# Kernel tuning notes

Hardware: AMD Instinct MI355X
Metric: run time of the kernel (lower is better)

## Reference

```python
import jax, jax.numpy as jnp
import numpy as np

KS = 7
DIM = 1024
HEADS = 16
B = 2048

def _rpb_index(ks):
    # Replicates the torch buffer: relative_position_index, shape [ks*ks, ks*ks]
    ch = np.arange(ks)
    coords = np.stack(np.meshgrid(ch, ch, indexing='ij')).reshape(2, -1)  # [2, N]
    rel = coords[:, :, None] - coords[:, None, :]                          # [2, N, N]
    rel = rel.transpose(1, 2, 0).copy()                                    # [N, N, 2]
    rel[:, :, 0] += ks - 1
    rel[:, :, 1] += ks - 1
    rel[:, :, 0] *= 2 * ks - 1
    idx = np.flipud(np.fliplr(rel.sum(-1)))
    return jnp.asarray(idx.copy())

def setup_inputs() -> dict:
    key = jax.random.key(0)
    ks = jax.random.split(key, 4)
    x = jax.random.normal(ks[0], (B, KS, KS, DIM), dtype=jnp.float32)
    qkv_w = jax.random.normal(ks[1], (3 * DIM, DIM), dtype=jnp.float32) * (DIM ** -0.5)
    qkv_b = jnp.zeros((3 * DIM,), dtype=jnp.float32)
    rpb = jax.random.normal(ks[2], (HEADS, 2 * KS - 1, 2 * KS - 1), dtype=jnp.float32) * 0.02
    proj_w = jax.random.normal(ks[3], (DIM, DIM), dtype=jnp.float32) * (DIM ** -0.5)
    proj_b = jnp.zeros((DIM,), dtype=jnp.float32)
    return {"x": x, "qkv_w": qkv_w, "qkv_b": qkv_b, "rpb": rpb, "proj_w": proj_w, "proj_b": proj_b}

def reference(x, qkv_w, qkv_b, rpb, proj_w, proj_b):
    Bn, H, W, C = x.shape
    ksz = H
    N = H * W
    heads = rpb.shape[0]
    hd = C // heads
    scale = hd ** -0.5
    idx = _rpb_index(ksz)  # [N, N] int

    qkv = x.reshape(Bn, N, C) @ qkv_w.T + qkv_b              # [B, N, 3C]
    qkv = qkv.reshape(Bn, N, 3, heads, hd).transpose(2, 0, 3, 1, 4)  # [3, B, h, N, hd]
    q, k, v = qkv[0] * scale, qkv[1], qkv[2]

    attn = jnp.einsum('bhnd,bhmd->bhnm', q, k)               # [B, h, N, N]
    # gather relative-position bias: rpb[h, 2k-1, 2k-1] -> flat [(2k-1)^2, h] -> [N, N, h]
    bias = rpb.transpose(1, 2, 0).reshape(-1, heads)[idx.reshape(-1)]
    bias = bias.reshape(N, N, heads).transpose(2, 0, 1)      # [h, N, N]
    attn = jax.nn.softmax(attn + bias[None], axis=-1)

    out = jnp.einsum('bhnm,bhmd->bhnd', attn, v)             # [B, h, N, hd]
    out = out.transpose(0, 2, 1, 3).reshape(Bn, H, W, C)
    return out @ proj_w.T + proj_b
```

## Files before the change

kernel.cpp:

```cpp
#include <hip/hip_runtime.h>


typedef _Float16 f16;
typedef _Float16 f16x8 __attribute__((ext_vector_type(8)));
typedef _Float16 f16x4 __attribute__((ext_vector_type(4)));
typedef float f32x4 __attribute__((ext_vector_type(4)));

#define G1P(p) ((const __attribute__((address_space(1))) unsigned int*)(p))
#define L3P(p) ((__attribute__((address_space(3))) unsigned int*)(p))

__global__ void cvt_kernel(const float* __restrict__ in, f16* __restrict__ out, int n4) {
  int i = blockIdx.x * blockDim.x + threadIdx.x;
  int stride = gridDim.x * blockDim.x;
  const float4* in4 = (const float4*)in;
  f16x4* out4 = (f16x4*)out;
  for (; i < n4; i += stride) {
    float4 v = in4[i];
    f16x4 o = { (f16)v.x, (f16)v.y, (f16)v.z, (f16)v.w };
    out4[i] = o;
  }
}

__global__ void bias_kernel(const float* __restrict__ rpb, f16* __restrict__ bias_t) {
  int h = blockIdx.x;
  for (int e = threadIdx.x; e < 4096; e += blockDim.x) {
    int m = e >> 6, n = e & 63;
    float v = -60000.f;
    if (n < 49 && m < 49) {
      int in_ = n / 7, jn = n % 7, im = m / 7, jm = m % 7;
      v = rpb[h * 169 + (im - in_ + 6) * 13 + (jm - jn + 6)] * 1.44269504f;
    }
    bias_t[h * 4096 + e] = (f16)v;
  }
}

#define VM4 asm volatile("s_waitcnt vmcnt(4)" ::: "memory")
#define VM0 asm volatile("s_waitcnt vmcnt(0)" ::: "memory")
#define NOVM ((void)0)
#define NOSTG ((void)0)

#define STAGE(GB, ROW0, COL0, LDSOFF)                                              \
  {                                                                                \
    const f16* s0_ = (GB) + (size_t)((ROW0) + wid * 32 + srow) * K + ((COL0) + sce); \
    __builtin_amdgcn_global_load_lds(G1P(s0_), L3P(lds + (LDSOFF) + wid * 2048), 16, 0, 0); \
    const f16* s1_ = s0_ + (size_t)16 * K;                                         \
    __builtin_amdgcn_global_load_lds(G1P(s1_), L3P(lds + (LDSOFF) + wid * 2048 + 1024), 16, 0, 0); \
  }

#define MFMA4(AREG, ROW)                                                           \
  acc[ROW][0] = __builtin_amdgcn_mfma_f32_16x16x32_f16(AREG, b0, acc[ROW][0], 0, 0, 0); \
  acc[ROW][1] = __builtin_amdgcn_mfma_f32_16x16x32_f16(AREG, b1, acc[ROW][1], 0, 0, 0); \
  acc[ROW][2] = __builtin_amdgcn_mfma_f32_16x16x32_f16(AREG, b2, acc[ROW][2], 0, 0, 0); \
  acc[ROW][3] = __builtin_amdgcn_mfma_f32_16x16x32_f16(AREG, b3, acc[ROW][3], 0, 0, 0);

#define PHASE(ABASE, BBASE, MH, STG, VMW)                                          \
  {                                                                                \
    f16x8 a0 = *(const f16x8*)((ABASE) + (wm * 128 + (MH) * 64 +  0 + l15) * 64 + swz); \
    f16x8 a1 = *(const f16x8*)((ABASE) + (wm * 128 + (MH) * 64 + 16 + l15) * 64 + swz); \
    f16x8 a2 = *(const f16x8*)((ABASE) + (wm * 128 + (MH) * 64 + 32 + l15) * 64 + swz); \
    f16x8 a3 = *(const f16x8*)((ABASE) + (wm * 128 + (MH) * 64 + 48 + l15) * 64 + swz); \
    if ((MH) == 0) {                                                               \
      b0 = *(const f16x8*)((BBASE) + (wn * 64 +  0 + l15) * 64 + swz);             \
      b1 = *(const f16x8*)((BBASE) + (wn * 64 + 16 + l15) * 64 + swz);             \
      b2 = *(const f16x8*)((BBASE) + (wn * 64 + 32 + l15) * 64 + swz);             \
      b3 = *(const f16x8*)((BBASE) + (wn * 64 + 48 + l15) * 64 + swz);             \
    }                                                                              \
    STG;                                                                           \
    __builtin_amdgcn_s_barrier();                                                  \
    asm volatile("s_waitcnt lgkmcnt(0)" ::: "memory");                             \
    __builtin_amdgcn_sched_barrier(0);                                             \
    __builtin_amdgcn_s_setprio(1);                                                 \
    MFMA4(a0, (MH) * 4 + 0) MFMA4(a1, (MH) * 4 + 1)                                \
    MFMA4(a2, (MH) * 4 + 2) MFMA4(a3, (MH) * 4 + 3)                                \
    __builtin_amdgcn_s_setprio(0);                                                 \
    VMW;                                                                           \
    __builtin_amdgcn_s_barrier();                                                  \
  }

template <typename OutT, bool HB>
__global__ __launch_bounds__(512, 2)
void gemm256(const f16* __restrict__ A, const f16* __restrict__ B,
             const float* __restrict__ bias, OutT* __restrict__ C,
             int N, int K, int ntiles_n) {
  __shared__ char lds[131072];
  const int tid = threadIdx.x;
  const int wid = tid >> 6, ln = tid & 63;
  const int l15 = ln & 15, lhi = ln >> 4;
  const int wm = wid >> 2, wn = wid & 3;
  const int srow = ln >> 2;
  const int sce = (((ln & 3) ^ ((ln >> 3) & 3)) << 3);
  const int swz = ((lhi ^ ((l15 >> 1) & 3)) << 4);

  const int nblk = gridDim.x;
  const int wg = (blockIdx.x & 7) * (nblk >> 3) + (blockIdx.x >> 3);
  const int bn = wg % ntiles_n, bm = wg / ntiles_n;
  const int m0 = bm * 256, n0 = bn * 256;

  f32x4 acc[8][4];
#pragma unroll
  for (int i = 0; i < 8; ++i)
#pragma unroll
    for (int j = 0; j < 4; ++j) acc[i][j] = (f32x4){0.f, 0.f, 0.f, 0.f};
  f16x8 b0, b1, b2, b3;

  STAGE(A, m0, 0, 0);
  STAGE(B, n0, 0, 32768);
  STAGE(A, m0, 32, 16384);
  STAGE(B, n0, 32, 49152);
  STAGE(A, m0, 64, 65536);
  STAGE(B, n0, 64, 98304);
  VM4;
  __builtin_amdgcn_s_barrier();

  for (int i = 0; i < 7; ++i) {
    const int cT1k1 = (2 * i + 1) * 64 + 32;
    const int cT2k0 = (2 * i + 2) * 64;
    const int cT2k1 = cT2k0 + 32;
    const int cT3k0 = (2 * i + 3) * 64;
    PHASE(lds + 0,      lds + 32768,  0, STAGE(A, m0, cT1k1, 81920),  NOVM);
    PHASE(lds + 0,      lds + 32768,  1, STAGE(B, n0, cT1k1, 114688), NOVM);
    PHASE(lds + 16384,  lds + 49152,  0, STAGE(A, m0, cT2k0, 0),      NOVM);
    PHASE(lds + 16384,  lds + 49152,  1, STAGE(B, n0, cT2k0, 32768),  VM4);
    PHASE(lds + 65536,  lds + 98304,  0, STAGE(A, m0, cT2k1, 16384),  NOVM);
    PHASE(lds + 65536,  lds + 98304,  1, STAGE(B, n0, cT2k1, 49152),  NOVM);
    PHASE(lds + 81920,  lds + 114688, 0, STAGE(A, m0, cT3k0, 65536),  NOVM);
    PHASE(lds + 81920,  lds + 114688, 1, STAGE(B, n0, cT3k0, 98304),  VM4);
  }
  PHASE(lds + 0,      lds + 32768,  0, STAGE(A, m0, 15 * 64 + 32, 81920),  NOVM);
  PHASE(lds + 0,      lds + 32768,  1, STAGE(B, n0, 15 * 64 + 32, 114688), NOVM);
  PHASE(lds + 16384,  lds + 49152,  0, NOSTG, NOVM);
  PHASE(lds + 16384,  lds + 49152,  1, NOSTG, VM0);
  PHASE(lds + 65536,  lds + 98304,  0, NOSTG, NOVM);
  PHASE(lds + 65536,  lds + 98304,  1, NOSTG, NOVM);
  PHASE(lds + 81920,  lds + 114688, 0, NOSTG, NOVM);
  PHASE(lds + 81920,  lds + 114688, 1, NOSTG, NOVM);

  float bv[4];
#pragma unroll
  for (int j = 0; j < 4; ++j) bv[j] = bias[n0 + wn * 64 + j * 16 + l15];
#pragma unroll
  for (int ii = 0; ii < 8; ++ii)
#pragma unroll
    for (int r = 0; r < 4; ++r) {
      int gr = m0 + wm * 128 + ii * 16 + lhi * 4 + r;
      if (HB) {
        int bw = gr / 49, n = gr - bw * 49;
#pragma unroll
        for (int j = 0; j < 4; ++j) {
          int gc = n0 + wn * 64 + j * 16 + l15;
          int which = gc >> 10, rem = gc & 1023;
          int h = rem >> 6, d = rem & 63;
          size_t addr = (((size_t)bw * 16 + h) * 3 + which) * 3136 + n * 64 + d;
          C[addr] = (OutT)(acc[ii][j][r] + bv[j]);
        }
      } else {
#pragma unroll
        for (int j = 0; j < 4; ++j) {
          int gc = n0 + wn * 64 + j * 16 + l15;
          C[(size_t)gr * N + gc] = (OutT)(acc[ii][j][r] + bv[j]);
        }
      }
    }
}

__global__ __launch_bounds__(64)
void attn_kernel(const f16* __restrict__ qkv,
                 const f16* __restrict__ bias_t,
                 f16* __restrict__ out) {
  __shared__ char lds[16384];
  const int bh = blockIdx.x;
  const int b = bh >> 4, h = bh & 15;
  const int ln = threadIdx.x;
  const int l15 = ln & 15, lhi = ln >> 4;
  const size_t base = (size_t)b * 49;
  const size_t qb = (size_t)bh * 3 * 3136;
  const size_t kb = qb + 3136;
  const size_t vb = qb + 6272;

  {
    int rA = ln >> 3, lc = ln & 7;
#pragma unroll
    for (int c = 0; c < 8; ++c) {
      int r = c * 8 + rA;
      int rc = r > 48 ? 48 : r;
      int ce = (lc ^ (r & 7)) << 3;
      const f16* g = qkv + kb + rc * 64 + ce;
      __builtin_amdgcn_global_load_lds(G1P(g), L3P(lds + c * 1024), 16, 0, 0);
    }
  }

  int rv = ln > 48 ? 48 : ln;
  const f16* vp = qkv + vb + rv * 64;
  f16x8 vr[8];
#pragma unroll
  for (int j = 0; j < 8; ++j) vr[j] = *(const f16x8*)(vp + j * 8);

  f16x8 qf[4][2];
#pragma unroll
  for (int t = 0; t < 4; ++t) {
    int rq = t * 16 + l15;
    if (rq > 48) rq = 48;
    const f16* qp = qkv + qb + rq * 64 + lhi * 8;
    qf[t][0] = *(const f16x8*)(qp);
    qf[t][1] = *(const f16x8*)(qp + 32);
  }

  const f16* bb = bias_t + h * 4096;
  f16x4 bq[4][4];
#pragma unroll
  for (int i = 0; i < 4; ++i)
#pragma unroll
    for (int j = 0; j < 4; ++j)
      bq[i][j] = *(const f16x4*)(bb + (j * 16 + l15) * 64 + i * 16 + lhi * 4);

#pragma unroll
  for (int d = 0; d < 64; ++d)
    *(f16*)(lds + 8192 + d * 128 + ((ln * 2) ^ ((d & 7) << 4))) = vr[d >> 3][d & 7];

  asm volatile("s_waitcnt vmcnt(0)" ::: "memory");
  __builtin_amdgcn_sched_barrier(0);

  f32x4 acc[4][4];
#pragma unroll
  for (int i = 0; i < 4; ++i)
#pragma unroll
    for (int j = 0; j < 4; ++j) acc[i][j] = (f32x4){0.f, 0.f, 0.f, 0.f};
#pragma unroll
  for (int kk = 0; kk < 2; ++kk) {
    f16x8 bf[4];
#pragma unroll
    for (int t = 0; t < 4; ++t) {
      int mr = t * 16 + l15;
      int pb = (kk * 64 + lhi * 16) ^ ((mr & 7) << 4);
      bf[t] = *(const f16x8*)(lds + mr * 128 + pb);
    }
    __builtin_amdgcn_s_setprio(1);
#pragma unroll
    for (int i = 0; i < 4; ++i)
#pragma unroll
      for (int j = 0; j < 4; ++j)
        acc[i][j] = __builtin_amdgcn_mfma_f32_16x16x32_f16(qf[i][kk], bf[j], acc[i][j], 0, 0, 0);
    __builtin_amdgcn_s_setprio(0);
  }

  const float SC = 0.125f * 1.44269504f;
#pragma unroll
  for (int i = 0; i < 4; ++i) {
#pragma unroll
    for (int r = 0; r < 4; ++r) {
      int n = i * 16 + lhi * 4 + r;
      float lv[4];
#pragma unroll
      for (int j = 0; j < 4; ++j)
        lv[j] = acc[i][j][r] * SC + (float)bq[i][j][r];
      float Mx = fmaxf(fmaxf(lv[0], lv[1]), fmaxf(lv[2], lv[3]));
#pragma unroll
      for (int off = 1; off < 16; off <<= 1) Mx = fmaxf(Mx, __shfl_xor(Mx, off));
      float s = 0.f;
#pragma unroll
      for (int j = 0; j < 4; ++j) { lv[j] = exp2f(lv[j] - Mx); s += lv[j]; }
#pragma unroll
      for (int off = 1; off < 16; off <<= 1) s += __shfl_xor(s, off);
      float inv = 1.f / s;
#pragma unroll
      for (int j = 0; j < 4; ++j) {
        int m = j * 16 + l15;
        *(f16*)(lds + n * 128 + ((m * 2) ^ ((n & 7) << 4))) = (f16)(lv[j] * inv);
      }
    }
  }

  f32x4 o[4][4];
#pragma unroll
  for (int i = 0; i < 4; ++i)
#pragma unroll
    for (int j = 0; j < 4; ++j) o[i][j] = (f32x4){0.f, 0.f, 0.f, 0.f};
#pragma unroll
  for (int kk = 0; kk < 2; ++kk) {
    f16x8 af[4], bf[4];
#pragma unroll
    for (int t = 0; t < 4; ++t) {
      int nr = t * 16 + l15;
      int pb = (kk * 64 + lhi * 16) ^ ((nr & 7) << 4);
      af[t] = *(const f16x8*)(lds + nr * 128 + pb);
      bf[t] = *(const f16x8*)(lds + 8192 + nr * 128 + pb);
    }
    __builtin_amdgcn_s_setprio(1);
#pragma unroll
    for (int i = 0; i < 4; ++i)
#pragma unroll
      for (int j = 0; j < 4; ++j)
        o[i][j] = __builtin_amdgcn_mfma_f32_16x16x32_f16(af[i], bf[j], o[i][j], 0, 0, 0);
    __builtin_amdgcn_s_setprio(0);
  }
#pragma unroll
  for (int i = 0; i < 4; ++i)
#pragma unroll
    for (int j = 0; j < 4; ++j)
#pragma unroll
      for (int r = 0; r < 4; ++r) {
        int n = i * 16 + lhi * 4 + r;
        if (n < 49)
          out[(base + n) * 1024 + h * 64 + j * 16 + l15] = (f16)o[i][j][r];
      }
}

extern "C" void kernel_launch(void* const* d_in, const int* in_sizes, int n_in,
                              void* d_out, int out_size, void* d_ws, size_t ws_size,
                              hipStream_t stream) {
  const float* x      = (const float*)d_in[0];
  const float* qkv_w  = (const float*)d_in[1];
  const float* qkv_b  = (const float*)d_in[2];
  const float* rpb    = (const float*)d_in[3];
  const float* proj_w = (const float*)d_in[4];
  const float* proj_b = (const float*)d_in[5];
  float* out = (float*)d_out;

  char* ws = (char*)d_ws;
  f16*   x16      = (f16*)(ws);
  f16*   wq16     = (f16*)(ws + 205520896);
  f16*   wp16     = (f16*)(ws + 211812352);
  f16*   qkv16    = (f16*)(ws + 213909504);
  f16*   attn16   = (f16*)(ws + 830472192);
  f16*   bias_t   = (f16*)(ws + 1035993088);

  cvt_kernel<<<2048, 256, 0, stream>>>(x, x16, 102760448 / 4);
  cvt_kernel<<<1024, 256, 0, stream>>>(qkv_w, wq16, 3145728 / 4);
  cvt_kernel<<<512, 256, 0, stream>>>(proj_w, wp16, 1048576 / 4);
  bias_kernel<<<16, 64, 0, stream>>>(rpb, bias_t);

  gemm256<f16, true><<<4704, 512, 0, stream>>>(x16, wq16, qkv_b, qkv16, 3072, 1024, 12);
  attn_kernel<<<2048 * 16, 64, 0, stream>>>(qkv16, bias_t, attn16);
  gemm256<float, false><<<1568, 512, 0, stream>>>(attn16, wp16, proj_b, out, 1024, 1024, 4);
}
```

Before: 1.252 ms.

## Store attention output head-blocked and gather it in projection GEMM loads

The attention kernel now writes each (batch, head) output as one contiguous 49x64 block instead of scattering rows into a token-major [B*49, 1024] layout. The projection GEMM's A-operand staging gains a head-blocked address mode that maps each (row, col) back into that layout. The goal is contiguous, coalesced stores from the attention kernel. The cost is index arithmetic (a divide by 49) in every A staging load and more scattered 16-byte global reads in the projection GEMM.

```diff
diff --git a/kernel.cpp b/kernel.cpp
--- a/kernel.cpp
+++ b/kernel.cpp
@@ -39,9 +39,27 @@
 #define NOVM ((void)0)
 #define NOSTG ((void)0)
 
-#define STAGE(GB, ROW0, COL0, LDSOFF)                                              \
+template <bool HBIN>
+__device__ __forceinline__ const f16* aptr(const f16* A, int row, int col, int K) {
+  if (HBIN) {
+    int bw = row / 49, n = row - bw * 49;
+    int h = col >> 6, d = col & 63;
+    return A + (size_t)bw * 50176 + h * 3136 + n * 64 + d;
+  }
+  return A + (size_t)row * K + col;
+}
+
+#define STAGEA(ROW0, COL0, LDSOFF)                                                 \
   {                                                                                \
-    const f16* s0_ = (GB) + (size_t)((ROW0) + wid * 32 + srow) * K + ((COL0) + sce); \
+    const f16* s0_ = aptr<HBIN>(A, (ROW0) + wid * 32 + srow, (COL0) + sce, K);     \
+    __builtin_amdgcn_global_load_lds(G1P(s0_), L3P(lds + (LDSOFF) + wid * 2048), 16, 0, 0); \
+    const f16* s1_ = aptr<HBIN>(A, (ROW0) + wid * 32 + srow + 16, (COL0) + sce, K); \
+    __builtin_amdgcn_global_load_lds(G1P(s1_), L3P(lds + (LDSOFF) + wid * 2048 + 1024), 16, 0, 0); \
+  }
+
+#define STAGEB(ROW0, COL0, LDSOFF)                                                 \
+  {                                                                                \
+    const f16* s0_ = B + (size_t)((ROW0) + wid * 32 + srow) * K + ((COL0) + sce);  \
     __builtin_amdgcn_global_load_lds(G1P(s0_), L3P(lds + (LDSOFF) + wid * 2048), 16, 0, 0); \
     const f16* s1_ = s0_ + (size_t)16 * K;                                         \
     __builtin_amdgcn_global_load_lds(G1P(s1_), L3P(lds + (LDSOFF) + wid * 2048 + 1024), 16, 0, 0); \
@@ -77,7 +95,7 @@
     __builtin_amdgcn_s_barrier();                                                  \
   }
 
-template <typename OutT, bool HB>
+template <typename OutT, bool HBOUT, bool HBIN>
 __global__ __launch_bounds__(512, 2)
 void gemm256(const f16* __restrict__ A, const f16* __restrict__ B,
              const float* __restrict__ bias, OutT* __restrict__ C,
@@ -103,12 +121,12 @@
     for (int j = 0; j < 4; ++j) acc[i][j] = (f32x4){0.f, 0.f, 0.f, 0.f};
   f16x8 b0, b1, b2, b3;
 
-  STAGE(A, m0, 0, 0);
-  STAGE(B, n0, 0, 32768);
-  STAGE(A, m0, 32, 16384);
-  STAGE(B, n0, 32, 49152);
-  STAGE(A, m0, 64, 65536);
-  STAGE(B, n0, 64, 98304);
+  STAGEA(m0, 0, 0);
+  STAGEB(n0, 0, 32768);
+  STAGEA(m0, 32, 16384);
+  STAGEB(n0, 32, 49152);
+  STAGEA(m0, 64, 65536);
+  STAGEB(n0, 64, 98304);
   VM4;
   __builtin_amdgcn_s_barrier();
 
@@ -117,17 +135,17 @@
     const int cT2k0 = (2 * i + 2) * 64;
     const int cT2k1 = cT2k0 + 32;
     const int cT3k0 = (2 * i + 3) * 64;
-    PHASE(lds + 0,      lds + 32768,  0, STAGE(A, m0, cT1k1, 81920),  NOVM);
-    PHASE(lds + 0,      lds + 32768,  1, STAGE(B, n0, cT1k1, 114688), NOVM);
-    PHASE(lds + 16384,  lds + 49152,  0, STAGE(A, m0, cT2k0, 0),      NOVM);
-    PHASE(lds + 16384,  lds + 49152,  1, STAGE(B, n0, cT2k0, 32768),  VM4);
-    PHASE(lds + 65536,  lds + 98304,  0, STAGE(A, m0, cT2k1, 16384),  NOVM);
-    PHASE(lds + 65536,  lds + 98304,  1, STAGE(B, n0, cT2k1, 49152),  NOVM);
-    PHASE(lds + 81920,  lds + 114688, 0, STAGE(A, m0, cT3k0, 65536),  NOVM);
-    PHASE(lds + 81920,  lds + 114688, 1, STAGE(B, n0, cT3k0, 98304),  VM4);
-  }
-  PHASE(lds + 0,      lds + 32768,  0, STAGE(A, m0, 15 * 64 + 32, 81920),  NOVM);
-  PHASE(lds + 0,      lds + 32768,  1, STAGE(B, n0, 15 * 64 + 32, 114688), NOVM);
+    PHASE(lds + 0,      lds + 32768,  0, STAGEA(m0, cT1k1, 81920),  NOVM);
+    PHASE(lds + 0,      lds + 32768,  1, STAGEB(n0, cT1k1, 114688), NOVM);
+    PHASE(lds + 16384,  lds + 49152,  0, STAGEA(m0, cT2k0, 0),      NOVM);
+    PHASE(lds + 16384,  lds + 49152,  1, STAGEB(n0, cT2k0, 32768),  VM4);
+    PHASE(lds + 65536,  lds + 98304,  0, STAGEA(m0, cT2k1, 16384),  NOVM);
+    PHASE(lds + 65536,  lds + 98304,  1, STAGEB(n0, cT2k1, 49152),  NOVM);
+    PHASE(lds + 81920,  lds + 114688, 0, STAGEA(m0, cT3k0, 65536),  NOVM);
+    PHASE(lds + 81920,  lds + 114688, 1, STAGEB(n0, cT3k0, 98304),  VM4);
+  }
+  PHASE(lds + 0,      lds + 32768,  0, STAGEA(m0, 15 * 64 + 32, 81920),  NOVM);
+  PHASE(lds + 0,      lds + 32768,  1, STAGEB(n0, 15 * 64 + 32, 114688), NOVM);
   PHASE(lds + 16384,  lds + 49152,  0, NOSTG, NOVM);
   PHASE(lds + 16384,  lds + 49152,  1, NOSTG, VM0);
   PHASE(lds + 65536,  lds + 98304,  0, NOSTG, NOVM);
@@ -143,7 +161,7 @@
 #pragma unroll
     for (int r = 0; r < 4; ++r) {
       int gr = m0 + wm * 128 + ii * 16 + lhi * 4 + r;
-      if (HB) {
+      if (HBOUT) {
         int bw = gr / 49, n = gr - bw * 49;
 #pragma unroll
         for (int j = 0; j < 4; ++j) {
@@ -169,10 +187,9 @@
                  f16* __restrict__ out) {
   __shared__ char lds[16384];
   const int bh = blockIdx.x;
-  const int b = bh >> 4, h = bh & 15;
+  const int h = bh & 15;
   const int ln = threadIdx.x;
   const int l15 = ln & 15, lhi = ln >> 4;
-  const size_t base = (size_t)b * 49;
   const size_t qb = (size_t)bh * 3 * 3136;
   const size_t kb = qb + 3136;
   const size_t vb = qb + 6272;
@@ -293,6 +310,7 @@
         o[i][j] = __builtin_amdgcn_mfma_f32_16x16x32_f16(af[i], bf[j], o[i][j], 0, 0, 0);
     __builtin_amdgcn_s_setprio(0);
   }
+  f16* ob = out + (size_t)bh * 3136;
 #pragma unroll
   for (int i = 0; i < 4; ++i)
 #pragma unroll
@@ -301,7 +319,7 @@
       for (int r = 0; r < 4; ++r) {
         int n = i * 16 + lhi * 4 + r;
         if (n < 49)
-          out[(base + n) * 1024 + h * 64 + j * 16 + l15] = (f16)o[i][j][r];
+          ob[n * 64 + j * 16 + l15] = (f16)o[i][j][r];
       }
 }
 
@@ -321,7 +339,7 @@
   f16*   wq16     = (f16*)(ws + 205520896);
   f16*   wp16     = (f16*)(ws + 211812352);
   f16*   qkv16    = (f16*)(ws + 213909504);
-  f16*   attn16   = (f16*)(ws + 830472192);
+  f16*   attnHB   = (f16*)(ws + 830472192);
   f16*   bias_t   = (f16*)(ws + 1035993088);
 
   cvt_kernel<<<2048, 256, 0, stream>>>(x, x16, 102760448 / 4);
@@ -329,7 +347,7 @@
   cvt_kernel<<<512, 256, 0, stream>>>(proj_w, wp16, 1048576 / 4);
   bias_kernel<<<16, 64, 0, stream>>>(rpb, bias_t);
 
-  gemm256<f16, true><<<4704, 512, 0, stream>>>(x16, wq16, qkv_b, qkv16, 3072, 1024, 12);
-  attn_kernel<<<2048 * 16, 64, 0, stream>>>(qkv16, bias_t, attn16);
-  gemm256<float, false><<<1568, 512, 0, stream>>>(attn16, wp16, proj_b, out, 1024, 1024, 4);
-}
+  gemm256<f16, true, false><<<4704, 512, 0, stream>>>(x16, wq16, qkv_b, qkv16, 3072, 1024, 12);
+  attn_kernel<<<2048 * 16, 64, 0, stream>>>(qkv16, bias_t, attnHB);
+  gemm256<float, false, true><<<1568, 512, 0, stream>>>(attnHB, wp16, proj_b, out, 1024, 1024, 4);
+}
```

Result: no change. 1.237 ms (-1.3%).
